# Optimization experiments

Hardware: AMD Instinct MI355X
Metric: run time of the kernel (lower is better)

## Reference

```python
import jax, jax.numpy as jnp
import numpy as np

B, F, S, P, E, H = 64, 32, 512, 96, 8, 2048
TOP_K = 2
ALPHA = 10.0
ENT_EPS = 1e-8
CV_EPS = 1e-10


def setup_inputs() -> dict:
    key = jax.random.key(0)
    ks = jax.random.split(key, 8)
    s = 0.02
    return {
        "x": jax.random.normal(ks[0], (B, F, S), dtype=jnp.float32),
        "time_embedding": jax.random.normal(ks[1], (B, F, S), dtype=jnp.float32),
        "Wg": jax.random.normal(ks[2], (S, E), dtype=jnp.float32) * s,
        "bg": jnp.zeros((E,), dtype=jnp.float32),
        "W1": jax.random.normal(ks[3], (E, S, H), dtype=jnp.float32) * s,
        "b1": jnp.zeros((E, H), dtype=jnp.float32),
        "W2": jax.random.normal(ks[4], (E, H, P), dtype=jnp.float32) * s,
        "b2": jnp.zeros((E, P), dtype=jnp.float32),
    }


def _gates(tf, Wg, bg):
    # tf: [F, B, S] -> logits [F, B, E]
    logits = jnp.einsum('fbs,se->fbe', tf, Wg) + bg
    # kthvalue(x, E - top_k + 1) = (E - top_k)-th entry (0-based) of ascending sort = k-th largest
    kth = jnp.sort(logits, axis=-1)[..., E - TOP_K]  # [F, B]
    mask = logits < kth[..., None]
    sm = jax.nn.softmax(logits, axis=-1)
    dec = jnp.where(mask, ALPHA * jnp.log(sm + 1.0), ALPHA * (jnp.exp(sm) - 1.0))
    return jax.nn.softmax(dec, axis=-1)  # [F, B, E]


def reference(x, time_embedding, Wg, bg, W1, b1, W2, b2):
    xf = jnp.transpose(x, (1, 0, 2))               # [F, B, S]
    tf = jnp.transpose(time_embedding, (1, 0, 2))  # [F, B, S]
    gates = _gates(tf, Wg, bg)                     # [F, B, E]

    # all experts on all features (eval mode: dropout = identity)
    h = jax.nn.gelu(jnp.einsum('fbs,esh->febh', xf, W1) + b1[None, :, None, :], approximate=False)
    eo = jnp.einsum('febh,ehp->febp', h, W2) + b2[None, :, None, :]  # [F, E, B, P]
    out = jnp.einsum('fbe,febp->fbp', gates, eo)   # gated weighted sum
    output = jnp.transpose(out, (1, 0, 2))         # [B, F, P]

    # selector loss: cv_squared of importance = gates.sum(batch) expanded over pred_len
    gsum = gates.sum(axis=1)                       # [F, E]
    imp = jnp.broadcast_to(gsum[..., None], (F, E, P)).reshape(F, E * P)
    cv = jnp.var(imp, axis=1, ddof=1) / (jnp.mean(imp, axis=1) ** 2 + CV_EPS)
    selector_loss = jnp.sum(cv)                    # loss_coef = 1.0

    # entropy loss: importance1 = gates.mean(batch) expanded over pred_len
    gmean = gates.mean(axis=1)                     # [F, E]
    imp1 = jnp.broadcast_to(gmean[..., None], (F, E, P))
    entropy_loss = jnp.sum((-imp1 * jnp.log(imp1 + ENT_EPS)).mean(axis=(1, 2)))

    return output, selector_loss, entropy_loss
```

## Files before the change

kernel.cpp:

```cpp
#include <hip/hip_runtime.h>
#include <math.h>

#define B_ 64
#define F_ 32
#define S_ 512
#define P_ 96
#define E_ 8
#define H_ 2048
#define M_ 2048

#define BM 128
#define BH 64
#define BK 64
#define ZSPLIT 4
#define HPZ (H_ / ZSPLIT)
#define NHT (HPZ / BH)
#define NKC (S_ / BK)

typedef __bf16 bf16x8 __attribute__((ext_vector_type(8)));
typedef __bf16 bf16x4 __attribute__((ext_vector_type(4)));
typedef float f32x4 __attribute__((ext_vector_type(4)));

#define MFMA16(a, b, c) __builtin_amdgcn_mfma_f32_16x16x32_bf16((a), (b), (c), 0, 0, 0)

#define GLL16(gp, lp) __builtin_amdgcn_global_load_lds(                     \
    (const __attribute__((address_space(1))) void*)(gp),                    \
    (__attribute__((address_space(3))) void*)(lp), 16, 0, 0)

__device__ __forceinline__ float fast_gelu(float x) {
  float e = __builtin_amdgcn_exp2f(-2.45546696f * x);
  return x * __builtin_amdgcn_rcpf(1.0f + e);
}

__global__ __launch_bounds__(256) void k_prep_w1(const float* __restrict__ W1,
                                                 __bf16* __restrict__ w1t) {
  __shared__ float tile[64 * 65];
  const int blk = blockIdx.x;
  const int tid = threadIdx.x;
  int e = blk >> 8, tt = blk & 255;
  int si = tt >> 5, hi = tt & 31;
  const float* src = W1 + (size_t)e * S_ * H_ + (size_t)(si * 64) * H_ + hi * 64;
  {
    int row = tid >> 2;
    int cb = (tid & 3) * 16;
#pragma unroll
    for (int k = 0; k < 4; ++k) {
      f32x4 v = *(const f32x4*)(src + (size_t)row * H_ + cb + k * 4);
#pragma unroll
      for (int u = 0; u < 4; ++u) tile[row * 65 + cb + k * 4 + u] = v[u];
    }
  }
  __syncthreads();
  {
    int h = tid >> 2;
    int sb = (tid & 3) * 16;
    __bf16* dst = w1t + (size_t)e * H_ * S_ + (size_t)(hi * 64 + h) * S_ + si * 64 + sb;
    bf16x8 o0, o1;
#pragma unroll
    for (int k = 0; k < 8; ++k) o0[k] = (__bf16)tile[(sb + k) * 65 + h];
#pragma unroll
    for (int k = 0; k < 8; ++k) o1[k] = (__bf16)tile[(sb + 8 + k) * 65 + h];
    *(bf16x8*)dst = o0;
    *(bf16x8*)(dst + 8) = o1;
  }
}

__global__ __launch_bounds__(256) void k_prep_rest(const float* __restrict__ x,
                                                   const float* __restrict__ te,
                                                   const float* __restrict__ Wg,
                                                   const float* __restrict__ bg,
                                                   const float* __restrict__ W2,
                                                   __bf16* __restrict__ xbf,
                                                   __bf16* __restrict__ w2t,
                                                   float* __restrict__ gates,
                                                   float* __restrict__ out) {
  __shared__ float tile[64 * 65];
  const int blk = blockIdx.x;
  const int tid = threadIdx.x;

  if (blk < 512) {
    int t = blk;
    int e = t >> 6, hi = (t >> 1) & 31, ph = t & 1;
    const float* src = W2 + (size_t)e * H_ * P_ + (size_t)(hi * 64) * P_ + ph * 48;
    {
      int h = tid & 63;
      int seg = tid >> 6;
#pragma unroll
      for (int k = 0; k < 3; ++k) {
        f32x4 v = *(const f32x4*)(src + (size_t)h * P_ + seg * 12 + k * 4);
#pragma unroll
        for (int u = 0; u < 4; ++u) tile[h * 49 + seg * 12 + k * 4 + u] = v[u];
      }
    }
    __syncthreads();
    if (tid < 192) {
      int p = tid >> 2;
      int hb = (tid & 3) * 16;
      __bf16* dst = w2t + (size_t)e * P_ * H_ + (size_t)(ph * 48 + p) * H_ + hi * 64 + hb;
      bf16x8 o0, o1;
#pragma unroll
      for (int k = 0; k < 8; ++k) o0[k] = (__bf16)tile[(hb + k) * 49 + p];
#pragma unroll
      for (int k = 0; k < 8; ++k) o1[k] = (__bf16)tile[(hb + 8 + k) * 49 + p];
      *(bf16x8*)dst = o0;
      *(bf16x8*)(dst + 8) = o1;
    }
    return;
  }
  if (blk < 1024) {
    size_t i = (size_t)(blk - 512) * 2048 + (size_t)tid * 8;
#pragma unroll
    for (int k = 0; k < 2; ++k) {
      f32x4 v = *(const f32x4*)(x + i + k * 4);
      bf16x4 o = {(__bf16)v[0], (__bf16)v[1], (__bf16)v[2], (__bf16)v[3]};
      *(bf16x4*)(xbf + i + k * 4) = o;
    }
    return;
  }
  if (blk < 1536) {
    int wave = tid >> 6, lane = tid & 63;
    int m = (blk - 1024) * 4 + wave;
    const float* trow = te + (size_t)m * S_;
    float acc[E_];
#pragma unroll
    for (int e = 0; e < E_; ++e) acc[e] = 0.f;
    for (int s = lane; s < S_; s += 64) {
      float t = trow[s];
      const f32x4* wgr = (const f32x4*)(Wg + s * E_);
      f32x4 a = wgr[0], b = wgr[1];
      acc[0] += t * a[0]; acc[1] += t * a[1]; acc[2] += t * a[2]; acc[3] += t * a[3];
      acc[4] += t * b[0]; acc[5] += t * b[1]; acc[6] += t * b[2]; acc[7] += t * b[3];
    }
#pragma unroll
    for (int e = 0; e < E_; ++e) {
#pragma unroll
      for (int off = 32; off > 0; off >>= 1) acc[e] += __shfl_xor(acc[e], off, 64);
    }
    if (lane == 0) {
      float lg[E_];
      float m1 = -3.4e38f, m2 = -3.4e38f;
#pragma unroll
      for (int e = 0; e < E_; ++e) {
        float v = acc[e] + bg[e];
        lg[e] = v;
        if (v > m1) { m2 = m1; m1 = v; }
        else if (v > m2) { m2 = v; }
      }
      float den = 0.f, sm[E_];
#pragma unroll
      for (int e = 0; e < E_; ++e) { sm[e] = expf(lg[e] - m1); den += sm[e]; }
      float inv = 1.f / den;
      float dmax = -3.4e38f, dec[E_];
#pragma unroll
      for (int e = 0; e < E_; ++e) {
        float p = sm[e] * inv;
        float d = (lg[e] < m2) ? (10.f * logf(p + 1.f)) : (10.f * (expf(p) - 1.f));
        dec[e] = d;
        dmax = fmaxf(dmax, d);
      }
      float dden = 0.f;
#pragma unroll
      for (int e = 0; e < E_; ++e) { dec[e] = expf(dec[e] - dmax); dden += dec[e]; }
      float dinv = 1.f / dden;
#pragma unroll
      for (int e = 0; e < E_; ++e) gates[m * E_ + e] = dec[e] * dinv;
    }
    return;
  }
  {
    size_t i = (size_t)(blk - 1536) * 1024 + (size_t)tid * 4;
    f32x4 z4 = {0.f, 0.f, 0.f, 0.f};
    *(f32x4*)(out + i) = z4;
  }
}

__global__ __launch_bounds__(512, 4) void k_experts(
    const __bf16* __restrict__ xbf,
    const __bf16* __restrict__ w1t,
    const __bf16* __restrict__ w2t,
    const float* __restrict__ b1,
    const float* __restrict__ b2,
    const float* __restrict__ gates,
    float* __restrict__ out)
{
  __shared__ __align__(16) __bf16 W1s[2][BH * BK];
  __shared__ __align__(16) __bf16 Xs[2][BM * BK];
  __shared__ __align__(16) __bf16 Hs[BM * BH];

  const int tid = threadIdx.x;

  if (blockIdx.z == ZSPLIT) {
    if (blockIdx.x != 0 || blockIdx.y != 0) return;
    float* gsum = (float*)&Xs[0][0];
    float* cvs  = gsum + F_ * E_;
    float* ents = cvs + F_;
    if (tid < 256) {
      int f = tid >> 3, ee = tid & 7;
      float s = 0.f;
      for (int b = 0; b < B_; ++b) s += gates[(size_t)(b * F_ + f) * E_ + ee];
      gsum[f * E_ + ee] = s;
    }
    __syncthreads();
    if (tid < F_) {
      float mean = 0.f;
#pragma unroll
      for (int k = 0; k < E_; ++k) mean += gsum[tid * E_ + k];
      mean *= (1.f / E_);
      float ss = 0.f;
#pragma unroll
      for (int k = 0; k < E_; ++k) { float d = gsum[tid * E_ + k] - mean; ss += d * d; }
      float var = (float)P_ * ss / (float)(E_ * P_ - 1);
      cvs[tid] = var / (mean * mean + 1e-10f);
      float ent = 0.f;
#pragma unroll
      for (int k = 0; k < E_; ++k) { float g = gsum[tid * E_ + k] * (1.f / B_); ent += -g * logf(g + 1e-8f); }
      ents[tid] = ent * (1.f / E_);
    }
    __syncthreads();
    if (tid == 0) {
      float a = 0.f, b = 0.f;
      for (int k = 0; k < F_; ++k) { a += cvs[k]; b += ents[k]; }
      out[(size_t)M_ * P_ + 0] = a;
      out[(size_t)M_ * P_ + 1] = b;
    }
    return;
  }

  const int wave = tid >> 6, lane = tid & 63;
  const int l15 = lane & 15, quad = lane >> 4;
  const int e = blockIdx.x;
  const int m0 = blockIdx.y * BM;
  const int hz = blockIdx.z * HPZ;

  const int sg = lane & 7;
  const int srl = lane >> 3;
  const int gcol = (sg ^ srl) * 8;

  const __bf16* w1base = w1t + ((size_t)e * H_ + hz + wave * 8 + srl) * S_ + gcol;
  const __bf16* xg = xbf + (size_t)(m0 + wave * 16 + srl) * S_ + gcol;
  const __bf16* w2z = w2t + (size_t)e * P_ * H_ + hz;

  const int hq = (wave & 1) * 32;
  const int mq = (wave >> 1) * 32;
  const int w16 = wave * 16;

  const f32x4 fz = {0.f, 0.f, 0.f, 0.f};
  f32x4 acc1[2][2];
  f32x4 acc2[6];
#pragma unroll
  for (int j = 0; j < 6; ++j) acc2[j] = fz;

  auto STAGE_W1 = [&](int slot, const __bf16* src) {
    GLL16(src, &W1s[slot][(wave * 8) * BK]);
  };
  auto STAGE_X = [&](int slot, const __bf16* src) {
#pragma unroll
    for (int p = 0; p < 2; ++p)
      GLL16(src + (size_t)(p * 8) * S_, &Xs[slot][(wave * 16 + p * 8) * BK]);
  };

  auto COMPUTE = [&](const __bf16* w1s, const __bf16* xs) {
#pragma unroll
    for (int kk = 0; kk < 2; ++kk) {
      bf16x8 af[2], bx[2];
#pragma unroll
      for (int i = 0; i < 2; ++i) {
        int r = hq + i * 16 + l15;
        af[i] = *(const bf16x8*)&w1s[r * BK + (((kk * 4 + quad) ^ (r & 7)) * 8)];
      }
#pragma unroll
      for (int j = 0; j < 2; ++j) {
        int r = mq + j * 16 + l15;
        bx[j] = *(const bf16x8*)&xs[r * BK + (((kk * 4 + quad) ^ (r & 7)) * 8)];
      }
#pragma unroll
      for (int i = 0; i < 2; ++i)
#pragma unroll
        for (int j = 0; j < 2; ++j)
          acc1[i][j] = MFMA16(af[i], bx[j], acc1[i][j]);
    }
  };

  auto GEMM2 = [&](int htc) {
    const __bf16* w2c = w2z + htc * BH;
#pragma unroll
    for (int kk = 0; kk < 2; ++kk) {
      int ab = (w16 + l15) * (BH * 2) + (((kk * 4 + quad) ^ (l15 & 7)) * 16);
      bf16x8 a = *(const bf16x8*)((const char*)Hs + ab);
#pragma unroll
      for (int j = 0; j < 6; ++j) {
        bf16x8 bb = *(const bf16x8*)(w2c + (size_t)(j * 16 + l15) * H_ + kk * 32 + quad * 8);
        acc2[j] = MFMA16(a, bb, acc2[j]);
      }
    }
  };

  auto GELU = [&](int ht_) {
    const float* b1w = b1 + (size_t)e * H_ + hz + ht_ * BH + hq;
#pragma unroll
    for (int i = 0; i < 2; ++i) {
      f32x4 bv = *(const f32x4*)(b1w + i * 16 + quad * 4);
#pragma unroll
      for (int j = 0; j < 2; ++j) {
        bf16x4 hv;
#pragma unroll
        for (int r = 0; r < 4; ++r)
          hv[r] = (__bf16)fast_gelu(acc1[i][j][r] + bv[r]);
        int m = mq + j * 16 + l15;
        int h = hq + i * 16 + quad * 4;
        int wb = (m * (BH * 2) + h * 2) ^ ((m & 7) << 4);
        *(bf16x4*)((char*)Hs + wb) = hv;
      }
    }
  };

  STAGE_W1(0, w1base);
  STAGE_X(0, xg);
  __syncthreads();

  for (int ht = 0; ht < NHT; ++ht) {
#pragma unroll
    for (int i = 0; i < 2; ++i)
#pragma unroll
      for (int j = 0; j < 2; ++j) acc1[i][j] = fz;

    const __bf16* w1h = w1base + (size_t)(ht * BH) * S_;

#pragma unroll
    for (int kc = 0; kc < NKC; ++kc) {
      if (kc < NKC - 1) {
        STAGE_W1((kc + 1) & 1, w1h + (kc + 1) * BK);
        STAGE_X((kc + 1) & 1, xg + (kc + 1) * BK);
      } else if (ht < NHT - 1) {
        STAGE_W1(0, w1h + (size_t)BH * S_);
        STAGE_X(0, xg);
      }
      if (kc == 0 && ht > 0) GEMM2(ht - 1);

      COMPUTE(&W1s[kc & 1][0], &Xs[kc & 1][0]);
      __syncthreads();
    }
    GELU(ht);
    __syncthreads();
  }
  GEMM2(NHT - 1);

#pragma unroll
  for (int r = 0; r < 4; ++r) {
    int m = m0 + w16 + quad * 4 + r;
    float g = gates[m * E_ + e];
#pragma unroll
    for (int j = 0; j < 6; ++j) {
      int col = j * 16 + l15;
      float v = acc2[j][r];
      if (blockIdx.z == 0) v += b2[e * P_ + col];
      atomicAdd(&out[(size_t)m * P_ + col], g * v);
    }
  }
}

extern "C" void kernel_launch(void* const* d_in, const int* in_sizes, int n_in,
                              void* d_out, int out_size, void* d_ws, size_t ws_size,
                              hipStream_t stream) {
  const float* x  = (const float*)d_in[0];
  const float* te = (const float*)d_in[1];
  const float* Wg = (const float*)d_in[2];
  const float* bg = (const float*)d_in[3];
  const float* W1 = (const float*)d_in[4];
  const float* b1 = (const float*)d_in[5];
  const float* W2 = (const float*)d_in[6];
  const float* b2 = (const float*)d_in[7];
  float* out = (float*)d_out;

  char* ws = (char*)d_ws;
  float* gates = (float*)ws;
  __bf16* xbf  = (__bf16*)(ws + 65536);
  __bf16* w1t  = (__bf16*)(ws + 65536 + 2097152);
  __bf16* w2t  = (__bf16*)(ws + 65536 + 2097152 + 16777216);

  k_prep_w1<<<2048, 256, 0, stream>>>(W1, w1t);
  k_prep_rest<<<1728, 256, 0, stream>>>(x, te, Wg, bg, W2, xbf, w2t, gates, out);
  k_experts<<<dim3(E_, M_ / BM, ZSPLIT + 1), 512, 0, stream>>>(xbf, w1t, w2t, b1, b2, gates, out);
}
```

Baseline: 210.8 us.

## Enlarge expert GEMM tiles to 128x128 and halve H split

Raises the hidden-tile and K-chunk sizes from 64 to 128 and cuts the H-dimension split from 4 to 2. The staging, LDS swizzle, MFMA fragment loops and H-buffer layout are rewritten to fit the larger tiles. The aim is more MFMA work per barrier and per LDS load, and half as many atomic adds into the output. In exchange LDS use per block roughly doubles, occupancy drops (the min-blocks launch bound is removed), and the grid has fewer blocks.

```diff
diff --git a/kernel.cpp b/kernel.cpp
--- a/kernel.cpp
+++ b/kernel.cpp
@@ -10,9 +10,9 @@
 #define M_ 2048
 
 #define BM 128
-#define BH 64
-#define BK 64
-#define ZSPLIT 4
+#define BH 128
+#define BK 128
+#define ZSPLIT 2
 #define HPZ (H_ / ZSPLIT)
 #define NHT (HPZ / BH)
 #define NKC (S_ / BK)
@@ -174,7 +174,7 @@
   }
 }
 
-__global__ __launch_bounds__(512, 4) void k_experts(
+__global__ __launch_bounds__(512) void k_experts(
     const __bf16* __restrict__ xbf,
     const __bf16* __restrict__ w1t,
     const __bf16* __restrict__ w2t,
@@ -232,49 +232,49 @@
   const int m0 = blockIdx.y * BM;
   const int hz = blockIdx.z * HPZ;
 
-  const int sg = lane & 7;
-  const int srl = lane >> 3;
-  const int gcol = (sg ^ srl) * 8;
-
-  const __bf16* w1base = w1t + ((size_t)e * H_ + hz + wave * 8 + srl) * S_ + gcol;
-  const __bf16* xg = xbf + (size_t)(m0 + wave * 16 + srl) * S_ + gcol;
-  const __bf16* w2z = w2t + (size_t)e * P_ * H_ + hz;
-
-  const int hq = (wave & 1) * 32;
+  const int sg4 = lane & 15;
+  const int sr4 = lane >> 4;
+  int sw[4];
+#pragma unroll
+  for (int p = 0; p < 4; ++p) sw[p] = (sg4 ^ (p * 4 + sr4)) * 8;
+
+  const __bf16* w1row = w1t + ((size_t)e * H_ + hz + wave * 16 + sr4) * S_;
+  const __bf16* xrow  = xbf + (size_t)(m0 + wave * 16 + sr4) * S_;
+  const __bf16* w2z   = w2t + (size_t)e * P_ * H_ + hz;
+
+  const int hq = (wave & 1) * 64;
   const int mq = (wave >> 1) * 32;
   const int w16 = wave * 16;
 
   const f32x4 fz = {0.f, 0.f, 0.f, 0.f};
-  f32x4 acc1[2][2];
+  f32x4 acc1[4][2];
   f32x4 acc2[6];
 #pragma unroll
   for (int j = 0; j < 6; ++j) acc2[j] = fz;
 
-  auto STAGE_W1 = [&](int slot, const __bf16* src) {
-    GLL16(src, &W1s[slot][(wave * 8) * BK]);
+  auto STAGE = [&](int slot, int ht_, int kc_) {
+    const __bf16* w1p = w1row + (size_t)(ht_ * BH) * S_ + kc_ * BK;
+    const __bf16* xp  = xrow + kc_ * BK;
+#pragma unroll
+    for (int p = 0; p < 4; ++p) {
+      GLL16(w1p + (size_t)(p * 4) * S_ + sw[p], &W1s[slot][(wave * 16 + p * 4) * BK]);
+      GLL16(xp  + (size_t)(p * 4) * S_ + sw[p], &Xs[slot][(wave * 16 + p * 4) * BK]);
+    }
   };
-  auto STAGE_X = [&](int slot, const __bf16* src) {
-#pragma unroll
-    for (int p = 0; p < 2; ++p)
-      GLL16(src + (size_t)(p * 8) * S_, &Xs[slot][(wave * 16 + p * 8) * BK]);
-  };
-
-  auto COMPUTE = [&](const __bf16* w1s, const __bf16* xs) {
-#pragma unroll
-    for (int kk = 0; kk < 2; ++kk) {
-      bf16x8 af[2], bx[2];
-#pragma unroll
-      for (int i = 0; i < 2; ++i) {
-        int r = hq + i * 16 + l15;
-        af[i] = *(const bf16x8*)&w1s[r * BK + (((kk * 4 + quad) ^ (r & 7)) * 8)];
-      }
-#pragma unroll
-      for (int j = 0; j < 2; ++j) {
-        int r = mq + j * 16 + l15;
-        bx[j] = *(const bf16x8*)&xs[r * BK + (((kk * 4 + quad) ^ (r & 7)) * 8)];
-      }
-#pragma unroll
-      for (int i = 0; i < 2; ++i)
+
+  auto COMPUTE = [&](int slot) {
+#pragma unroll
+    for (int kk = 0; kk < 4; ++kk) {
+      const int gq = (((kk * 4 + quad) ^ l15) * 8);
+      bf16x8 af[4], bx[2];
+#pragma unroll
+      for (int i = 0; i < 4; ++i)
+        af[i] = *(const bf16x8*)&W1s[slot][(hq + i * 16 + l15) * BK + gq];
+#pragma unroll
+      for (int j = 0; j < 2; ++j)
+        bx[j] = *(const bf16x8*)&Xs[slot][(mq + j * 16 + l15) * BK + gq];
+#pragma unroll
+      for (int i = 0; i < 4; ++i)
 #pragma unroll
         for (int j = 0; j < 2; ++j)
           acc1[i][j] = MFMA16(af[i], bx[j], acc1[i][j]);
@@ -284,8 +284,8 @@
   auto GEMM2 = [&](int htc) {
     const __bf16* w2c = w2z + htc * BH;
 #pragma unroll
-    for (int kk = 0; kk < 2; ++kk) {
-      int ab = (w16 + l15) * (BH * 2) + (((kk * 4 + quad) ^ (l15 & 7)) * 16);
+    for (int kk = 0; kk < 4; ++kk) {
+      int ab = (w16 + l15) * 256 + (((kk * 4 + quad) ^ l15) * 16);
       bf16x8 a = *(const bf16x8*)((const char*)Hs + ab);
 #pragma unroll
       for (int j = 0; j < 6; ++j) {
@@ -296,10 +296,11 @@
   };
 
   auto GELU = [&](int ht_) {
-    const float* b1w = b1 + (size_t)e * H_ + hz + ht_ * BH + hq;
-#pragma unroll
-    for (int i = 0; i < 2; ++i) {
-      f32x4 bv = *(const f32x4*)(b1w + i * 16 + quad * 4);
+    const float* b1w = b1 + (size_t)e * H_ + hz + ht_ * BH;
+#pragma unroll
+    for (int i = 0; i < 4; ++i) {
+      int h = hq + i * 16 + quad * 4;
+      f32x4 bv = *(const f32x4*)(b1w + h);
 #pragma unroll
       for (int j = 0; j < 2; ++j) {
         bf16x4 hv;
@@ -307,37 +308,31 @@
         for (int r = 0; r < 4; ++r)
           hv[r] = (__bf16)fast_gelu(acc1[i][j][r] + bv[r]);
         int m = mq + j * 16 + l15;
-        int h = hq + i * 16 + quad * 4;
-        int wb = (m * (BH * 2) + h * 2) ^ ((m & 7) << 4);
+        int wb = m * 256 + (((h >> 3) ^ l15) * 16) + (quad & 1) * 8;
         *(bf16x4*)((char*)Hs + wb) = hv;
       }
     }
   };
 
-  STAGE_W1(0, w1base);
-  STAGE_X(0, xg);
+  STAGE(0, 0, 0);
   __syncthreads();
 
   for (int ht = 0; ht < NHT; ++ht) {
 #pragma unroll
-    for (int i = 0; i < 2; ++i)
+    for (int i = 0; i < 4; ++i)
 #pragma unroll
       for (int j = 0; j < 2; ++j) acc1[i][j] = fz;
-
-    const __bf16* w1h = w1base + (size_t)(ht * BH) * S_;
 
 #pragma unroll
     for (int kc = 0; kc < NKC; ++kc) {
       if (kc < NKC - 1) {
-        STAGE_W1((kc + 1) & 1, w1h + (kc + 1) * BK);
-        STAGE_X((kc + 1) & 1, xg + (kc + 1) * BK);
+        STAGE((kc + 1) & 1, ht, kc + 1);
       } else if (ht < NHT - 1) {
-        STAGE_W1(0, w1h + (size_t)BH * S_);
-        STAGE_X(0, xg);
+        STAGE(0, ht + 1, 0);
       }
       if (kc == 0 && ht > 0) GEMM2(ht - 1);
 
-      COMPUTE(&W1s[kc & 1][0], &Xs[kc & 1][0]);
+      COMPUTE(kc & 1);
       __syncthreads();
     }
     GELU(ht);
```

Measured after the change: 214.6 us. About the same (+1.8%).
